# Kernel tuning notes

Measured on AMD Instinct MI355X. Metric: run time of the kernel, lower is better.

Reference implementation:

```python
import jax, jax.numpy as jnp
import numpy as np

V = 20000   # input_size (POI vocab)
U = 10000   # user_count
H = 128     # hidden_size
B = 64      # user_len (batch)
S = 200     # seq_len
LAM_T = 0.01
LAM_S = 100.0
DAY = 86400.0


def setup_inputs() -> dict:
    key = jax.random.key(0)
    ks = jax.random.split(key, 12)
    sc = 1.0 / np.sqrt(H)
    return {
        "poi_inputs": jax.random.randint(ks[0], (B, S), 0, V),
        "lengths": jnp.full((B,), S, dtype=jnp.int32),  # full sequences -> pack/pad is identity
        "timestamp_inputs": jnp.sort(jax.random.uniform(ks[1], (B, S), minval=0.0, maxval=DAY), axis=1),
        "location_inputs": jax.random.normal(ks[2], (B, S, 2)) * 0.1,
        "active_user": jax.random.randint(ks[3], (B,), 0, U),
        "emb_W": jax.random.normal(ks[4], (V, H)),      # nn.Embedding default N(0,1)
        "user_W": jax.random.normal(ks[5], (U, H)),
        "W_ih": jax.random.uniform(ks[6], (H, H), minval=-sc, maxval=sc),
        "W_hh": jax.random.uniform(ks[7], (H, H), minval=-sc, maxval=sc),
        "b_ih": jax.random.uniform(ks[8], (H,), minval=-sc, maxval=sc),
        "b_hh": jax.random.uniform(ks[9], (H,), minval=-sc, maxval=sc),
        "fc_W": jax.random.uniform(ks[10], (V, 2 * H), minval=-sc, maxval=sc),  # torch Linear [out,in]
        "fc_b": jax.random.uniform(ks[11], (V,), minval=-sc, maxval=sc),
    }


def _safe_norm(d):
    # norm over last axis with zero (not nan) gradient at d == 0
    d2 = jnp.sum(d * d, axis=-1)
    pos = d2 > 0
    return jnp.where(pos, jnp.sqrt(jnp.where(pos, d2, 1.0)), 0.0)


def reference(poi_inputs, lengths, timestamp_inputs, location_inputs, active_user,
              emb_W, user_W, W_ih, W_hh, b_ih, b_hh, fc_W, fc_b):
    t, s = timestamp_inputs, location_inputs
    x_emb = emb_W[poi_inputs]                       # [B,S,H]

    # vanilla tanh RNN (torch nn.RNN, batch_first) via scan over time
    def step(h, xt):
        h = jnp.tanh(xt @ W_ih.T + b_ih + h @ W_hh.T + b_hh)
        return h, h
    h0 = jnp.zeros((x_emb.shape[0], W_hh.shape[0]), x_emb.dtype)
    _, out = jax.lax.scan(step, h0, jnp.swapaxes(x_emb, 0, 1))
    out = jnp.swapaxes(out, 0, 1)                   # [B,S,H]

    # vectorized spatio-temporal decay attention (original O(S^2) python loop)
    dt = jnp.maximum(t[:, :, None] - t[:, None, :], 0.0)          # [B,S,S] clamp_min(0)
    ds = _safe_norm(s[:, :, None, :] - s[:, None, :, :])          # [B,S,S]
    a_j = ((jnp.cos(dt * (2.0 * jnp.pi / DAY)) + 1.0) * 0.5) * jnp.exp(-dt * LAM_T)
    b_j = jnp.exp(-ds * LAM_S)
    causal = jnp.tril(jnp.ones((t.shape[1], t.shape[1]), bool))   # j <= i
    w = jnp.where(causal, a_j * b_j + 1e-10, 0.0)                 # [B,S,S]
    sum_w = jnp.maximum(jnp.sum(w, axis=-1), 1e-10)               # [B,S]
    out_w = jnp.einsum('bij,bjh->bih', w, out) / sum_w[..., None] # [B,S,H]

    p_u = jnp.broadcast_to(user_W[active_user][:, None, :], out_w.shape)
    out_pu = jnp.concatenate([out_w, p_u], axis=-1)               # [B,S,2H]
    y = jax.nn.softmax(out_pu @ fc_W.T + fc_b, axis=-1)           # [B,S,V]
    return y, out_pu
```

## Files before the change

kernel.cpp:

```cpp
#include <hip/hip_runtime.h>
#include <hip/hip_bf16.h>
#include <stdint.h>

#define B_   64
#define S_   200
#define H_   128
#define V_   20000
#define M_   12800
#define NPAD 20224
#define NBN  158
#define NBM  100
#define NWG2 15800

#define WS_A      0u
#define WS_FCW    3276800u
#define WS_U      8454144u
#define WS_RSUM   13631488u
#define WS_WTIH   13682688u

#define XP_OFF    0
#define HOUT_OFF  2000000
#define PART_OFF  4000000
#define OUTPU_OFF 256000000ll

typedef __attribute__((ext_vector_type(8))) __bf16 bf16x8;
typedef __attribute__((ext_vector_type(4))) float  f32x4;

__device__ __forceinline__ void gll16(const void* g, void* l) {
  __builtin_amdgcn_global_load_lds(
      (const __attribute__((address_space(1))) void*)g,
      (__attribute__((address_space(3))) void*)l, 16, 0, 0);
}

__global__ __launch_bounds__(256)
void prep_w1(const float* __restrict__ fcw, __hip_bfloat16* __restrict__ w1) {
  int t = threadIdx.x;
  int row = blockIdx.x * 2 + (t >> 7);
  int col = t & 127;
  float v = (row < V_) ? fcw[(long)row * 256 + col] : 0.f;
  w1[(long)row * 128 + col] = __float2bfloat16(v);
}

__global__ __launch_bounds__(128)
void prep_wt(const float* __restrict__ w_ih, float* __restrict__ wt) {
  int bid = blockIdx.x, t = threadIdx.x;
  wt[bid * 128 + t] = w_ih[t * 128 + bid];
}

__global__ __launch_bounds__(256)
void user_k(const int* __restrict__ auser, const float* __restrict__ userW,
            const float* __restrict__ fcW, const float* __restrict__ fcb,
            float* __restrict__ U) {
  __shared__ float uw[8][128];
  int t = threadIdx.x;
  int c = blockIdx.x * 256 + t;
  int b0 = blockIdx.y * 8;
  for (int i = t; i < 8 * 128; i += 256) {
    int bb = i >> 7, kk = i & 127;
    uw[bb][kk] = userW[(long)auser[b0 + bb] * 128 + kk];
  }
  __syncthreads();
  float acc[8];
#pragma unroll
  for (int bb = 0; bb < 8; ++bb) acc[bb] = 0.f;
  if (c < V_) {
    const float* w2 = fcW + (long)c * 256 + 128;
#pragma unroll 4
    for (int k = 0; k < 128; k += 4) {
      float4 wv = *(const float4*)(w2 + k);
#pragma unroll
      for (int bb = 0; bb < 8; ++bb) {
        acc[bb] = fmaf(wv.x, uw[bb][k], acc[bb]);
        acc[bb] = fmaf(wv.y, uw[bb][k + 1], acc[bb]);
        acc[bb] = fmaf(wv.z, uw[bb][k + 2], acc[bb]);
        acc[bb] = fmaf(wv.w, uw[bb][k + 3], acc[bb]);
      }
    }
    float base = fcb[c];
#pragma unroll
    for (int bb = 0; bb < 8; ++bb)
      U[(long)(b0 + bb) * NPAD + c] = base + acc[bb];
  } else {
#pragma unroll
    for (int bb = 0; bb < 8; ++bb)
      U[(long)(b0 + bb) * NPAD + c] = -1e30f;
  }
}

__global__ __launch_bounds__(128)
void xproj_k(const int* __restrict__ poi, const float* __restrict__ emb,
             const float* __restrict__ wt_ih, const float* __restrict__ b_ih,
             const float* __restrict__ b_hh, float* __restrict__ xp) {
  __shared__ float xs[128];
  int m = blockIdx.x, j = threadIdx.x;
  xs[j] = emb[(long)poi[m] * 128 + j];
  __syncthreads();
  float acc = b_ih[j] + b_hh[j];
#pragma unroll 8
  for (int k = 0; k < 128; ++k) acc = fmaf(xs[k], wt_ih[k * 128 + j], acc);
  xp[(long)m * 128 + j] = acc;
}

__global__ __launch_bounds__(128)
void rnn_k(const float* __restrict__ xp, const float* __restrict__ w_hh,
           float* __restrict__ hout) {
  int b = blockIdx.x, j = threadIdx.x;
  float w[128];
#pragma unroll
  for (int k = 0; k < 128; ++k) w[k] = w_hh[j * 128 + k];
  __shared__ float hs[2][128];
  hs[0][j] = 0.f;
  __syncthreads();
  int cur = 0;
  for (int t = 0; t < S_; ++t) {
    float x0 = xp[((long)b * S_ + t) * 128 + j];
    const float* hp = hs[cur];
    float a0 = 0.f, a1 = 0.f, a2 = 0.f, a3 = 0.f;
#pragma unroll
    for (int k = 0; k < 32; ++k) {
      a0 = fmaf(hp[k],      w[k],      a0);
      a1 = fmaf(hp[k + 32], w[k + 32], a1);
      a2 = fmaf(hp[k + 64], w[k + 64], a2);
      a3 = fmaf(hp[k + 96], w[k + 96], a3);
    }
    float hn = tanhf(x0 + ((a0 + a1) + (a2 + a3)));
    hs[cur ^ 1][j] = hn;
    hout[((long)b * S_ + t) * 128 + j] = hn;
    cur ^= 1;
    __syncthreads();
  }
}

__global__ __launch_bounds__(128)
void attn_k(const float* __restrict__ ts, const float* __restrict__ loc,
            const float* __restrict__ hout, const int* __restrict__ auser,
            const float* __restrict__ userW, float* __restrict__ outpu,
            __hip_bfloat16* __restrict__ Abf) {
  int i = blockIdx.x, b = blockIdx.y, h = threadIdx.x;
  __shared__ float wl[128];
  const float OMEGA = 7.27220521664304e-05f;
  float ti = ts[b * S_ + i];
  float lx = loc[(b * S_ + i) * 2 + 0];
  float ly = loc[(b * S_ + i) * 2 + 1];
  float acc = 0.f, sw = 0.f;
  for (int jc = 0; jc <= i; jc += 128) {
    int j = jc + h;
    float wj = 0.f;
    if (j <= i) {
      float dt = fmaxf(ti - ts[b * S_ + j], 0.f);
      float a = (cosf(dt * OMEGA) + 1.f) * 0.5f * expf(-dt * 0.01f);
      float dx = lx - loc[(b * S_ + j) * 2 + 0];
      float dy = ly - loc[(b * S_ + j) * 2 + 1];
      float dn = sqrtf(dx * dx + dy * dy);
      wj = a * expf(-dn * 100.f) + 1e-10f;
    }
    __syncthreads();
    wl[h] = wj;
    __syncthreads();
    int lim = min(128, i - jc + 1);
    const float* hb = hout + ((long)b * S_ + jc) * 128 + h;
    for (int jj = 0; jj < lim; ++jj) {
      float wv = wl[jj];
      acc = fmaf(wv, hb[(long)jj * 128], acc);
      sw += wv;
    }
  }
  float ow = acc / fmaxf(sw, 1e-10f);
  long m = (long)b * S_ + i;
  float pu = userW[(long)auser[b] * 128 + h];
  outpu[m * 256 + h]       = ow;
  outpu[m * 256 + 128 + h] = pu;
  Abf[m * 128 + h]         = __float2bfloat16(ow);
}

template <int PASS>
__global__ __launch_bounds__(256)
void gemm_fc(const __hip_bfloat16* __restrict__ A,
             const __hip_bfloat16* __restrict__ Bw,
             const float* __restrict__ Ut,
             const float* __restrict__ rowsum,
             float* __restrict__ part,
             float* __restrict__ y) {
  __shared__ __align__(16) char smem[32768];
  __shared__ float rsum2[2][128];
  char* AsB = smem;
  char* BsB = smem + 8192;
  float* lbuf = (float*)smem;

  const int tid  = threadIdx.x;
  const int lane = tid & 63;
  const int wid  = tid >> 6;
  const int wr = wid >> 1, wc = wid & 1;
  const int g = lane >> 4, lr = lane & 15;

  const int orig = blockIdx.x;
  const int nid = (orig & 7) * (NWG2 / 8) + (orig >> 3);
  const int bn = nid / NBM, bm = nid % NBM;
  const long brow = (long)bm * 128, bcol = (long)bn * 128;

  f32x4 acc[4][4];
#pragma unroll
  for (int mi = 0; mi < 4; ++mi)
#pragma unroll
    for (int ni = 0; ni < 4; ++ni) acc[mi][ni] = (f32x4)(0.f);

  const char* Ab = (const char*)A + brow * 256;
  const char* Bb = (const char*)Bw + bcol * 256;
  const int c0 = tid, c1 = tid + 256;
  const int r0 = c0 >> 2, o0 = (c0 & 3) * 16;
  const int r1 = c1 >> 2, o1 = (c1 & 3) * 16;

  for (int kk = 0; kk < 4; ++kk) {
    __syncthreads();
    const int kb = kk * 64;
    gll16(Ab + (long)r0 * 256 + kb + o0, AsB + c0 * 16);
    gll16(Ab + (long)r1 * 256 + kb + o1, AsB + c1 * 16);
    gll16(Bb + (long)r0 * 256 + kb + o0, BsB + c0 * 16);
    gll16(Bb + (long)r1 * 256 + kb + o1, BsB + c1 * 16);
    __syncthreads();
    bf16x8 af[4], bfr[4];
#pragma unroll
    for (int mi = 0; mi < 4; ++mi)
      af[mi] = *(const bf16x8*)(AsB + (wr * 64 + mi * 16 + lr) * 64 + g * 16);
#pragma unroll
    for (int ni = 0; ni < 4; ++ni)
      bfr[ni] = *(const bf16x8*)(BsB + (wc * 64 + ni * 16 + lr) * 64 + g * 16);
#pragma unroll
    for (int mi = 0; mi < 4; ++mi)
#pragma unroll
      for (int ni = 0; ni < 4; ++ni)
        acc[mi][ni] = __builtin_amdgcn_mfma_f32_16x16x32_bf16(af[mi], bfr[ni], acc[mi][ni], 0, 0, 0);
  }

  if (PASS == 0) {
#pragma unroll
    for (int mi = 0; mi < 4; ++mi) {
#pragma unroll
      for (int r = 0; r < 4; ++r) {
        long row = brow + wr * 64 + mi * 16 + g * 4 + r;
        const float* urow = Ut + (long)(row / S_) * NPAD + bcol;
        float s = 0.f;
#pragma unroll
        for (int ni = 0; ni < 4; ++ni) {
          float u = urow[wc * 64 + ni * 16 + lr];
          s += __expf(acc[mi][ni][r] + u);
        }
#pragma unroll
        for (int off = 1; off < 16; off <<= 1) s += __shfl_xor(s, off);
        if (lr == 0) rsum2[wc][wr * 64 + mi * 16 + g * 4 + r] = s;
      }
    }
    __syncthreads();
    if (tid < 128)
      part[(long)bn * M_ + brow + tid] = rsum2[0][tid] + rsum2[1][tid];
  } else {
    if (bcol >= V_) return;
    const bool full = (bcol + 128 <= V_);
#pragma unroll
    for (int half = 0; half < 2; ++half) {
      __syncthreads();
      if (wr == half) {
#pragma unroll
        for (int mi = 0; mi < 4; ++mi) {
#pragma unroll
          for (int r = 0; r < 4; ++r) {
            int lrow = mi * 16 + g * 4 + r;
            long row = brow + half * 64 + lrow;
            const float* urow = Ut + (long)(row / S_) * NPAD + bcol;
            float inv = 1.0f / rowsum[row];
#pragma unroll
            for (int ni = 0; ni < 4; ++ni) {
              int lcol = wc * 64 + ni * 16 + lr;
              lbuf[lrow * 128 + lcol] = __expf(acc[mi][ni][r] + urow[lcol]) * inv;
            }
          }
        }
      }
      __syncthreads();
      if (full) {
#pragma unroll
        for (int it = 0; it < 8; ++it) {
          int idx = it * 256 + tid;
          int lrow = idx >> 5, c4 = idx & 31;
          long row = brow + half * 64 + lrow;
          *(float4*)(y + row * (long)V_ + bcol + c4 * 4) = ((const float4*)lbuf)[idx];
        }
      } else {
#pragma unroll
        for (int it = 0; it < 8; ++it) {
          int idx = it * 256 + tid;
          int lrow = idx >> 5, c4 = idx & 31;
          long row = brow + half * 64 + lrow;
#pragma unroll
          for (int e = 0; e < 4; ++e) {
            int col = (int)bcol + c4 * 4 + e;
            if (col < V_) y[row * (long)V_ + col] = lbuf[lrow * 128 + c4 * 4 + e];
          }
        }
      }
    }
  }
}

__global__ void reduce_rows(const float* __restrict__ part, float* __restrict__ rowsum) {
  int m = blockIdx.x * 256 + threadIdx.x;
  if (m < M_) {
    float s = 0.f;
    for (int bn = 0; bn < NBN; ++bn) s += part[(long)bn * M_ + m];
    rowsum[m] = fmaxf(s, 1e-30f);
  }
}

extern "C" void kernel_launch(void* const* d_in, const int* in_sizes, int n_in,
                              void* d_out, int out_size, void* d_ws, size_t ws_size,
                              hipStream_t stream) {
  const int*   poi   = (const int*)d_in[0];
  const float* ts    = (const float*)d_in[2];
  const float* loc   = (const float*)d_in[3];
  const int*   auser = (const int*)d_in[4];
  const float* embW  = (const float*)d_in[5];
  const float* userW = (const float*)d_in[6];
  const float* w_ih  = (const float*)d_in[7];
  const float* w_hh  = (const float*)d_in[8];
  const float* b_ih  = (const float*)d_in[9];
  const float* b_hh  = (const float*)d_in[10];
  const float* fcW   = (const float*)d_in[11];
  const float* fcb   = (const float*)d_in[12];

  float* out = (float*)d_out;
  char*  ws  = (char*)d_ws;
  __hip_bfloat16* Abf    = (__hip_bfloat16*)(ws + WS_A);
  __hip_bfloat16* w1b    = (__hip_bfloat16*)(ws + WS_FCW);
  float*          Ut     = (float*)(ws + WS_U);
  float*          rowsum = (float*)(ws + WS_RSUM);
  float*          wt_ih  = (float*)(ws + WS_WTIH);

  float* xp    = out + XP_OFF;
  float* hout  = out + HOUT_OFF;
  float* part  = out + PART_OFF;
  float* outpu = out + OUTPU_OFF;

  prep_w1<<<dim3(NPAD / 2), dim3(256), 0, stream>>>(fcW, w1b);
  prep_wt<<<dim3(128), dim3(128), 0, stream>>>(w_ih, wt_ih);
  user_k<<<dim3(NPAD / 256, 8), dim3(256), 0, stream>>>(auser, userW, fcW, fcb, Ut);
  xproj_k<<<dim3(M_), dim3(128), 0, stream>>>(poi, embW, wt_ih, b_ih, b_hh, xp);
  rnn_k<<<dim3(B_), dim3(128), 0, stream>>>(xp, w_hh, hout);
  attn_k<<<dim3(S_, B_), dim3(128), 0, stream>>>(ts, loc, hout, auser, userW, outpu, Abf);
  gemm_fc<0><<<dim3(NWG2), dim3(256), 0, stream>>>(Abf, w1b, Ut, nullptr, part, nullptr);
  reduce_rows<<<dim3(50), dim3(256), 0, stream>>>(part, rowsum);
  gemm_fc<1><<<dim3(NWG2), dim3(256), 0, stream>>>(Abf, w1b, Ut, rowsum, nullptr, out);
}
```

Before: 828.2 us.

## Batch xproj rows, vectorize RNN reads, widen FC GEMM to 512 threads with swizzled LDS

xproj now computes 16 rows per block, so each W_ih column load is reused across 16 tokens. The RNN inner product reads hidden state as float4 from LDS. The FC GEMM kernels move to 512 threads (8 waves, 4x2 warp grid) and load the full K=256 tile into 64KB of LDS at once with an XOR swizzle to avoid bank conflicts, removing the per-k-step barriers. The softmax write pass handles all 128 rows in one swizzled staging buffer and uses nontemporal stores. The larger LDS footprint may limit how many blocks fit per CU.

```diff
diff --git a/kernel.cpp b/kernel.cpp
--- a/kernel.cpp
+++ b/kernel.cpp
@@ -91,14 +91,34 @@
 void xproj_k(const int* __restrict__ poi, const float* __restrict__ emb,
              const float* __restrict__ wt_ih, const float* __restrict__ b_ih,
              const float* __restrict__ b_hh, float* __restrict__ xp) {
-  __shared__ float xs[128];
-  int m = blockIdx.x, j = threadIdx.x;
-  xs[j] = emb[(long)poi[m] * 128 + j];
+  __shared__ float xs[16][128];
+  int j = threadIdx.x;
+  int m0 = blockIdx.x * 16;
+#pragma unroll
+  for (int i = 0; i < 16; ++i)
+    xs[i][j] = emb[(long)poi[m0 + i] * 128 + j];
   __syncthreads();
-  float acc = b_ih[j] + b_hh[j];
-#pragma unroll 8
-  for (int k = 0; k < 128; ++k) acc = fmaf(xs[k], wt_ih[k * 128 + j], acc);
-  xp[(long)m * 128 + j] = acc;
+  float bias = b_ih[j] + b_hh[j];
+  float acc[16];
+#pragma unroll
+  for (int i = 0; i < 16; ++i) acc[i] = bias;
+  for (int kq = 0; kq < 32; ++kq) {
+    float w0 = wt_ih[(4 * kq + 0) * 128 + j];
+    float w1 = wt_ih[(4 * kq + 1) * 128 + j];
+    float w2 = wt_ih[(4 * kq + 2) * 128 + j];
+    float w3 = wt_ih[(4 * kq + 3) * 128 + j];
+#pragma unroll
+    for (int i = 0; i < 16; ++i) {
+      float4 xv = *(const float4*)&xs[i][4 * kq];
+      acc[i] = fmaf(xv.x, w0, acc[i]);
+      acc[i] = fmaf(xv.y, w1, acc[i]);
+      acc[i] = fmaf(xv.z, w2, acc[i]);
+      acc[i] = fmaf(xv.w, w3, acc[i]);
+    }
+  }
+#pragma unroll
+  for (int i = 0; i < 16; ++i)
+    xp[(long)(m0 + i) * 128 + j] = acc[i];
 }
 
 __global__ __launch_bounds__(128)
@@ -114,14 +134,19 @@
   int cur = 0;
   for (int t = 0; t < S_; ++t) {
     float x0 = xp[((long)b * S_ + t) * 128 + j];
-    const float* hp = hs[cur];
+    const float4* hp4 = (const float4*)hs[cur];
     float a0 = 0.f, a1 = 0.f, a2 = 0.f, a3 = 0.f;
 #pragma unroll
-    for (int k = 0; k < 32; ++k) {
-      a0 = fmaf(hp[k],      w[k],      a0);
-      a1 = fmaf(hp[k + 32], w[k + 32], a1);
-      a2 = fmaf(hp[k + 64], w[k + 64], a2);
-      a3 = fmaf(hp[k + 96], w[k + 96], a3);
+    for (int k = 0; k < 8; ++k) {
+      float4 v0 = hp4[k], v1 = hp4[k + 8], v2 = hp4[k + 16], v3 = hp4[k + 24];
+      a0 = fmaf(v0.x, w[4 * k + 0], a0); a0 = fmaf(v0.y, w[4 * k + 1], a0);
+      a0 = fmaf(v0.z, w[4 * k + 2], a0); a0 = fmaf(v0.w, w[4 * k + 3], a0);
+      a1 = fmaf(v1.x, w[32 + 4 * k + 0], a1); a1 = fmaf(v1.y, w[32 + 4 * k + 1], a1);
+      a1 = fmaf(v1.z, w[32 + 4 * k + 2], a1); a1 = fmaf(v1.w, w[32 + 4 * k + 3], a1);
+      a2 = fmaf(v2.x, w[64 + 4 * k + 0], a2); a2 = fmaf(v2.y, w[64 + 4 * k + 1], a2);
+      a2 = fmaf(v2.z, w[64 + 4 * k + 2], a2); a2 = fmaf(v2.w, w[64 + 4 * k + 3], a2);
+      a3 = fmaf(v3.x, w[96 + 4 * k + 0], a3); a3 = fmaf(v3.y, w[96 + 4 * k + 1], a3);
+      a3 = fmaf(v3.z, w[96 + 4 * k + 2], a3); a3 = fmaf(v3.w, w[96 + 4 * k + 3], a3);
     }
     float hn = tanhf(x0 + ((a0 + a1) + (a2 + a3)));
     hs[cur ^ 1][j] = hn;
@@ -174,23 +199,23 @@
 }
 
 template <int PASS>
-__global__ __launch_bounds__(256)
+__global__ __launch_bounds__(512, 4)
 void gemm_fc(const __hip_bfloat16* __restrict__ A,
              const __hip_bfloat16* __restrict__ Bw,
              const float* __restrict__ Ut,
              const float* __restrict__ rowsum,
              float* __restrict__ part,
              float* __restrict__ y) {
-  __shared__ __align__(16) char smem[32768];
-  __shared__ float rsum2[2][128];
+  __shared__ __align__(16) char smem[65536];
+  __shared__ float rsum4[4][128];
   char* AsB = smem;
-  char* BsB = smem + 8192;
+  char* BsB = smem + 32768;
   float* lbuf = (float*)smem;
 
   const int tid  = threadIdx.x;
   const int lane = tid & 63;
   const int wid  = tid >> 6;
-  const int wr = wid >> 1, wc = wid & 1;
+  const int wr = wid >> 2, wc = wid & 3;
   const int g = lane >> 4, lr = lane & 15;
 
   const int orig = blockIdx.x;
@@ -198,37 +223,45 @@
   const int bn = nid / NBM, bm = nid % NBM;
   const long brow = (long)bm * 128, bcol = (long)bn * 128;
 
-  f32x4 acc[4][4];
-#pragma unroll
-  for (int mi = 0; mi < 4; ++mi)
-#pragma unroll
-    for (int ni = 0; ni < 4; ++ni) acc[mi][ni] = (f32x4)(0.f);
-
   const char* Ab = (const char*)A + brow * 256;
   const char* Bb = (const char*)Bw + bcol * 256;
-  const int c0 = tid, c1 = tid + 256;
-  const int r0 = c0 >> 2, o0 = (c0 & 3) * 16;
-  const int r1 = c1 >> 2, o1 = (c1 & 3) * 16;
-
+
+#pragma unroll
+  for (int i = 0; i < 4; ++i) {
+    int ci = i * 512 + tid;
+    int row = ci >> 4;
+    int w = (ci & 15) ^ (row & 7);
+    long src = (long)row * 256 + (long)w * 16;
+    gll16(Ab + src, AsB + (long)ci * 16);
+    gll16(Bb + src, BsB + (long)ci * 16);
+  }
+  __syncthreads();
+
+  f32x4 acc[4][2];
+#pragma unroll
+  for (int mi = 0; mi < 4; ++mi)
+#pragma unroll
+    for (int ni = 0; ni < 2; ++ni) acc[mi][ni] = (f32x4)(0.f);
+
+#pragma unroll
   for (int kk = 0; kk < 4; ++kk) {
-    __syncthreads();
-    const int kb = kk * 64;
-    gll16(Ab + (long)r0 * 256 + kb + o0, AsB + c0 * 16);
-    gll16(Ab + (long)r1 * 256 + kb + o1, AsB + c1 * 16);
-    gll16(Bb + (long)r0 * 256 + kb + o0, BsB + c0 * 16);
-    gll16(Bb + (long)r1 * 256 + kb + o1, BsB + c1 * 16);
-    __syncthreads();
-    bf16x8 af[4], bfr[4];
+    bf16x8 af[4], bfr[2];
+#pragma unroll
+    for (int mi = 0; mi < 4; ++mi) {
+      int row = wr * 64 + mi * 16 + lr;
+      int w = ((kk << 2) | g) ^ (row & 7);
+      af[mi] = *(const bf16x8*)(AsB + row * 256 + w * 16);
+    }
+#pragma unroll
+    for (int ni = 0; ni < 2; ++ni) {
+      int row = wc * 32 + ni * 16 + lr;
+      int w = ((kk << 2) | g) ^ (row & 7);
+      bfr[ni] = *(const bf16x8*)(BsB + row * 256 + w * 16);
+    }
 #pragma unroll
     for (int mi = 0; mi < 4; ++mi)
-      af[mi] = *(const bf16x8*)(AsB + (wr * 64 + mi * 16 + lr) * 64 + g * 16);
-#pragma unroll
-    for (int ni = 0; ni < 4; ++ni)
-      bfr[ni] = *(const bf16x8*)(BsB + (wc * 64 + ni * 16 + lr) * 64 + g * 16);
-#pragma unroll
-    for (int mi = 0; mi < 4; ++mi)
-#pragma unroll
-      for (int ni = 0; ni < 4; ++ni)
+#pragma unroll
+      for (int ni = 0; ni < 2; ++ni)
         acc[mi][ni] = __builtin_amdgcn_mfma_f32_16x16x32_bf16(af[mi], bfr[ni], acc[mi][ni], 0, 0, 0);
   }
 
@@ -241,61 +274,62 @@
         const float* urow = Ut + (long)(row / S_) * NPAD + bcol;
         float s = 0.f;
 #pragma unroll
-        for (int ni = 0; ni < 4; ++ni) {
-          float u = urow[wc * 64 + ni * 16 + lr];
+        for (int ni = 0; ni < 2; ++ni) {
+          float u = urow[wc * 32 + ni * 16 + lr];
           s += __expf(acc[mi][ni][r] + u);
         }
 #pragma unroll
         for (int off = 1; off < 16; off <<= 1) s += __shfl_xor(s, off);
-        if (lr == 0) rsum2[wc][wr * 64 + mi * 16 + g * 4 + r] = s;
+        if (lr == 0) rsum4[wc][wr * 64 + mi * 16 + g * 4 + r] = s;
       }
     }
     __syncthreads();
     if (tid < 128)
-      part[(long)bn * M_ + brow + tid] = rsum2[0][tid] + rsum2[1][tid];
+      part[(long)bn * M_ + brow + tid] =
+          rsum4[0][tid] + rsum4[1][tid] + rsum4[2][tid] + rsum4[3][tid];
   } else {
     if (bcol >= V_) return;
     const bool full = (bcol + 128 <= V_);
-#pragma unroll
-    for (int half = 0; half < 2; ++half) {
-      __syncthreads();
-      if (wr == half) {
-#pragma unroll
-        for (int mi = 0; mi < 4; ++mi) {
-#pragma unroll
-          for (int r = 0; r < 4; ++r) {
-            int lrow = mi * 16 + g * 4 + r;
-            long row = brow + half * 64 + lrow;
-            const float* urow = Ut + (long)(row / S_) * NPAD + bcol;
-            float inv = 1.0f / rowsum[row];
-#pragma unroll
-            for (int ni = 0; ni < 4; ++ni) {
-              int lcol = wc * 64 + ni * 16 + lr;
-              lbuf[lrow * 128 + lcol] = __expf(acc[mi][ni][r] + urow[lcol]) * inv;
-            }
-          }
+    __syncthreads();
+#pragma unroll
+    for (int mi = 0; mi < 4; ++mi) {
+#pragma unroll
+      for (int r = 0; r < 4; ++r) {
+        int lrow = wr * 64 + mi * 16 + g * 4 + r;
+        long row = brow + lrow;
+        const float* urow = Ut + (long)(row / S_) * NPAD + bcol;
+        float inv = 1.0f / rowsum[row];
+        int key = ((lrow >> 2) & 3) << 2;
+#pragma unroll
+        for (int ni = 0; ni < 2; ++ni) {
+          int lcol = wc * 32 + ni * 16 + lr;
+          lbuf[lrow * 128 + (lcol ^ key)] = __expf(acc[mi][ni][r] + urow[lcol]) * inv;
         }
       }
-      __syncthreads();
-      if (full) {
-#pragma unroll
-        for (int it = 0; it < 8; ++it) {
-          int idx = it * 256 + tid;
-          int lrow = idx >> 5, c4 = idx & 31;
-          long row = brow + half * 64 + lrow;
-          *(float4*)(y + row * (long)V_ + bcol + c4 * 4) = ((const float4*)lbuf)[idx];
-        }
-      } else {
-#pragma unroll
-        for (int it = 0; it < 8; ++it) {
-          int idx = it * 256 + tid;
-          int lrow = idx >> 5, c4 = idx & 31;
-          long row = brow + half * 64 + lrow;
-#pragma unroll
-          for (int e = 0; e < 4; ++e) {
-            int col = (int)bcol + c4 * 4 + e;
-            if (col < V_) y[row * (long)V_ + col] = lbuf[lrow * 128 + c4 * 4 + e];
-          }
+    }
+    __syncthreads();
+    if (full) {
+#pragma unroll
+      for (int it = 0; it < 8; ++it) {
+        int idx = it * 512 + tid;
+        int lrow = idx >> 5, c4 = idx & 31;
+        int key = ((lrow >> 2) & 3) << 2;
+        f32x4 v = *(const f32x4*)(lbuf + lrow * 128 + ((c4 * 4) ^ key));
+        __builtin_nontemporal_store(v,
+            (f32x4*)(y + (brow + lrow) * (long)V_ + bcol + c4 * 4));
+      }
+    } else {
+#pragma unroll
+      for (int it = 0; it < 8; ++it) {
+        int idx = it * 512 + tid;
+        int lrow = idx >> 5, c4 = idx & 31;
+        int key = ((lrow >> 2) & 3) << 2;
+        const float* src = lbuf + lrow * 128 + ((c4 * 4) ^ key);
+        long row = brow + lrow;
+#pragma unroll
+        for (int e = 0; e < 4; ++e) {
+          int col = (int)bcol + c4 * 4 + e;
+          if (col < V_) y[row * (long)V_ + col] = src[e];
         }
       }
     }
@@ -343,10 +377,10 @@
   prep_w1<<<dim3(NPAD / 2), dim3(256), 0, stream>>>(fcW, w1b);
   prep_wt<<<dim3(128), dim3(128), 0, stream>>>(w_ih, wt_ih);
   user_k<<<dim3(NPAD / 256, 8), dim3(256), 0, stream>>>(auser, userW, fcW, fcb, Ut);
-  xproj_k<<<dim3(M_), dim3(128), 0, stream>>>(poi, embW, wt_ih, b_ih, b_hh, xp);
+  xproj_k<<<dim3(M_ / 16), dim3(128), 0, stream>>>(poi, embW, wt_ih, b_ih, b_hh, xp);
   rnn_k<<<dim3(B_), dim3(128), 0, stream>>>(xp, w_hh, hout);
   attn_k<<<dim3(S_, B_), dim3(128), 0, stream>>>(ts, loc, hout, auser, userW, outpu, Abf);
-  gemm_fc<0><<<dim3(NWG2), dim3(256), 0, stream>>>(Abf, w1b, Ut, nullptr, part, nullptr);
+  gemm_fc<0><<<dim3(NWG2), dim3(512), 0, stream>>>(Abf, w1b, Ut, nullptr, part, nullptr);
   reduce_rows<<<dim3(50), dim3(256), 0, stream>>>(part, rowsum);
-  gemm_fc<1><<<dim3(NWG2), dim3(256), 0, stream>>>(Abf, w1b, Ut, rowsum, nullptr, out);
-}
+  gemm_fc<1><<<dim3(NWG2), dim3(512), 0, stream>>>(Abf, w1b, Ut, rowsum, nullptr, out);
+}
```

Measured after the change: 737.2 us. 11.0% less time.
